# Kernel tuning notes

Hardware: AMD Instinct MI355X
Metric: run time of the kernel (lower is better)

The kernel has to match this reference:

```python
import jax, jax.numpy as jnp
import numpy as np

N_HEADS = 16
N_KV_HEADS = 4
HEAD_DIM = 64
ROPE_BASE = 10000.0

def _rope_cos_sin(T, dtype):
    # flash-attn style: cos/sin of shape [T, head_dim//2]
    inv_freq = 1.0 / (ROPE_BASE ** (jnp.arange(0, HEAD_DIM, 2, dtype=jnp.float32) / HEAD_DIM))
    freqs = jnp.arange(T, dtype=jnp.float32)[:, None] * inv_freq[None, :]  # [T, D/2]
    return jnp.cos(freqs).astype(dtype), jnp.sin(freqs).astype(dtype)

def _apply_rope(x, cos, sin):
    # x: [B, H, T, D], non-interleaved rotate-half on full head dim
    d2 = HEAD_DIM // 2
    x1, x2 = x[..., :d2], x[..., d2:]
    c = cos[None, None, :, :]
    s = sin[None, None, :, :]
    return jnp.concatenate([x1 * c - x2 * s, x2 * c + x1 * s], axis=-1)

def setup_inputs() -> dict:
    key = jax.random.key(0)
    ks = jax.random.split(key, 6)
    B, T, D = 1, 4096, 1024
    def g(k, shape, scale):
        return jax.random.normal(k, shape, dtype=jnp.float32) * scale
    return {
        "query": g(ks[0], (B, T, D), 1.0),
        "Wq": g(ks[1], (D, D), D ** -0.5),
        "Wk": g(ks[2], (D, N_KV_HEADS * HEAD_DIM), D ** -0.5),
        "Wv": g(ks[3], (D, N_KV_HEADS * HEAD_DIM), D ** -0.5),
        "W1": g(ks[4], (D, 4 * D), D ** -0.5),
        "W2": g(ks[5], (4 * D, D), (4 * D) ** -0.5),
    }

def reference(query, Wq, Wk, Wv, W1, W2):
    B, T, D = query.shape
    # QKV projections -> [B, H, T, Dh]
    q = (query @ Wq).reshape(B, T, N_HEADS, HEAD_DIM).transpose(0, 2, 1, 3)
    k = (query @ Wk).reshape(B, T, N_KV_HEADS, HEAD_DIM).transpose(0, 2, 1, 3)
    v = (query @ Wv).reshape(B, T, N_KV_HEADS, HEAD_DIM).transpose(0, 2, 1, 3)
    # RoPE (seqlen_offset = 0, no cache)
    cos, sin = _rope_cos_sin(T, q.dtype)
    q = _apply_rope(q, cos, sin)
    k = _apply_rope(k, cos, sin)
    # GQA: repeat KV heads to match Q heads
    n_rep = N_HEADS // N_KV_HEADS
    k = jnp.repeat(k, n_rep, axis=1)
    v = jnp.repeat(v, n_rep, axis=1)
    # Scaled dot-product attention, causal
    scale = HEAD_DIM ** -0.5
    scores = jnp.einsum("bhqd,bhkd->bhqk", q, k) * scale
    i = jnp.arange(T)[:, None]
    j = jnp.arange(T)[None, :]
    scores = jnp.where(j > i, jnp.finfo(scores.dtype).min, scores)
    attn = jax.nn.softmax(scores, axis=-1)
    out = jnp.einsum("bhqk,bhkd->bhqd", attn, v)  # [B, H, T, Dh]
    out = out.transpose(0, 2, 1, 3).reshape(B, T, D)
    # out_proj: Linear -> SiLU -> Linear (use_swiglu=True path)
    return jax.nn.silu(out @ W1) @ W2
```

## Files before the change

kernel.cpp:

```cpp
#include <hip/hip_runtime.h>
#include <stdint.h>

typedef unsigned short u16;
typedef __bf16 bf16x8 __attribute__((ext_vector_type(8)));
typedef float f32x4 __attribute__((ext_vector_type(4)));

#define T_SEQ 4096
#define DMODEL 1024

__device__ __forceinline__ float bf2f(u16 x) {
  union { uint32_t u; float f; } v; v.u = ((uint32_t)x) << 16; return v.f;
}
__device__ __forceinline__ u16 f2bf(float f) {
  union { float f; uint32_t u; } v; v.f = f;
  return (u16)((v.u + 0x7FFFu + ((v.u >> 16) & 1u)) >> 16);
}
__device__ __forceinline__ float fexp2(float x) {
#if __has_builtin(__builtin_amdgcn_exp2f)
  return __builtin_amdgcn_exp2f(x);
#else
  return __expf(x * 0.6931471805599453f);
#endif
}
__device__ __forceinline__ uint32_t pack_bf16(float lo, float hi) {
#if __has_builtin(__builtin_amdgcn_cvt_pk_bf16_f32)
  typedef __bf16 bf16x2_t __attribute__((ext_vector_type(2)));
  union { bf16x2_t v; uint32_t u; } c;
  c.v = __builtin_amdgcn_cvt_pk_bf16_f32(lo, hi);
  return c.u;
#else
  union { float f; uint32_t u; } a, b;
  a.f = lo; b.f = hi;
  return __builtin_amdgcn_perm(b.u + 0x8000u, a.u + 0x8000u, 0x07060302u);
#endif
}
__device__ __forceinline__ void async16(void* lds, const void* g) {
  __builtin_amdgcn_global_load_lds(
      (__attribute__((address_space(1))) void*)const_cast<void*>(g),
      (__attribute__((address_space(3))) void*)lds, 16, 0, 0);
}
__device__ __forceinline__ void storeC(u16* C, size_t i, float v) { C[i] = f2bf(v); }
__device__ __forceinline__ void storeC(float* C, size_t i, float v) { C[i] = v; }

__device__ __forceinline__ void wtrans_body(const float* __restrict__ in,
                                            u16* __restrict__ out, int K, int N,
                                            int bx, int by, int tid,
                                            float (*tile)[65]) {
  const int n0 = bx * 64, k0 = by * 64;
  const int r = tid >> 2, c = (tid & 3) * 16;
#pragma unroll
  for (int j = 0; j < 4; ++j) {
    float4 v = *(const float4*)&in[(size_t)(k0 + r) * N + n0 + c + j * 4];
    tile[r][c + j * 4 + 0] = v.x; tile[r][c + j * 4 + 1] = v.y;
    tile[r][c + j * 4 + 2] = v.z; tile[r][c + j * 4 + 3] = v.w;
  }
  __syncthreads();
  union { u16 s[16]; uint4 q[2]; } buf;
#pragma unroll
  for (int j = 0; j < 16; ++j) buf.s[j] = f2bf(tile[c + j][r]);
  u16* dst = out + (size_t)(n0 + r) * K + k0 + c;
  *(uint4*)(dst) = buf.q[0];
  *(uint4*)(dst + 8) = buf.q[1];
}

__global__ void __launch_bounds__(256) prep(const float* __restrict__ query,
                                            const float* __restrict__ Wq,
                                            const float* __restrict__ Wk,
                                            const float* __restrict__ Wv,
                                            const float* __restrict__ W1,
                                            const float* __restrict__ W2,
                                            u16* __restrict__ Xb,
                                            u16* __restrict__ WqkvT,
                                            u16* __restrict__ W1T,
                                            u16* __restrict__ W2T) {
  __shared__ float tile[64][65];
  const int b = blockIdx.x, tid = threadIdx.x;
  if (b < 4096) {
    int idx = (b * 256 + tid) * 4;
    float4 v = *(const float4*)(query + idx);
    union { u16 s[4]; uint2 q; } o;
    o.s[0] = f2bf(v.x); o.s[1] = f2bf(v.y); o.s[2] = f2bf(v.z); o.s[3] = f2bf(v.w);
    *(uint2*)(Xb + idx) = o.q;
  } else if (b < 4352) {
    int t = b - 4096;
    wtrans_body(Wq, WqkvT, 1024, 1024, t & 15, t >> 4, tid, tile);
  } else if (b < 4416) {
    int t = b - 4352;
    wtrans_body(Wk, WqkvT + (size_t)1024 * 1024, 1024, 256, t & 3, t >> 2, tid, tile);
  } else if (b < 4480) {
    int t = b - 4416;
    wtrans_body(Wv, WqkvT + (size_t)1280 * 1024, 1024, 256, t & 3, t >> 2, tid, tile);
  } else if (b < 5504) {
    int t = b - 4480;
    wtrans_body(W1, W1T, 1024, 4096, t & 63, t >> 6, tid, tile);
  } else {
    int t = b - 5504;
    wtrans_body(W2, W2T, 4096, 1024, t & 15, t >> 4, tid, tile);
  }
}

__global__ void __launch_bounds__(256) rope_vt(const u16* __restrict__ qkv,
                                               u16* __restrict__ Q,
                                               u16* __restrict__ Ko,
                                               u16* __restrict__ Vt) {
  __shared__ u16 tile[64][65];
  const int b = blockIdx.x, tid = threadIdx.x;
  if (b < 4096) {
    const int t = b;
    const int i = tid & 31;
    const float ang = (float)t * powf(10000.f, -(float)i * (1.f / 32.f));
    float s, c;
    sincosf(ang, &s, &c);
    const u16* row = qkv + (size_t)t * 1536;
    const float QS = 0.125f * 1.4426950408889634f;
    const float cq = c * QS, sq = s * QS;
#pragma unroll
    for (int it = 0; it < 2; ++it) {
      int h = (tid >> 5) + it * 8;
      float x1 = bf2f(row[h * 64 + i]);
      float x2 = bf2f(row[h * 64 + 32 + i]);
      size_t o = ((size_t)h * T_SEQ + t) * 64 + i;
      Q[o] = f2bf(x1 * cq - x2 * sq);
      Q[o + 32] = f2bf(x2 * cq + x1 * sq);
    }
    if (tid < 128) {
      int h = tid >> 5;
      float x1 = bf2f(row[1024 + h * 64 + i]);
      float x2 = bf2f(row[1024 + h * 64 + 32 + i]);
      size_t o = ((size_t)h * T_SEQ + t) * 64 + i;
      Ko[o] = f2bf(x1 * c - x2 * s);
      Ko[o + 32] = f2bf(x2 * c + x1 * s);
    }
  } else {
    const int t = b - 4096;
    const int t0 = (t & 63) * 64, h = t >> 6;
    const int r = tid >> 2, q4 = (tid & 3) * 16;
    const u16* src = qkv + (size_t)(t0 + r) * 1536 + 1280 + h * 64 + q4;
    union { u16 s[16]; uint4 q[2]; } buf;
    buf.q[0] = *(const uint4*)(src);
    buf.q[1] = *(const uint4*)(src + 8);
#pragma unroll
    for (int j = 0; j < 16; ++j) tile[r][q4 + j] = buf.s[j];
    __syncthreads();
#pragma unroll
    for (int j = 0; j < 16; ++j) buf.s[j] = tile[q4 + j][r];
    u16* dst = Vt + ((size_t)h * 64 + r) * T_SEQ + t0 + q4;
    *(uint4*)(dst) = buf.q[0];
    *(uint4*)(dst + 8) = buf.q[1];
  }
}

template <int AM, int ACT, typename OutT>
__global__ void __launch_bounds__(256) gemm_bt(const u16* __restrict__ A,
                                               const u16* __restrict__ Bt,
                                               OutT* __restrict__ C,
                                               int M, int N, int K) {
  __shared__ u16 sA[2][AM * 32][64];
  __shared__ u16 sB[2][128][64];
  const int tid = threadIdx.x;
  const int w = tid >> 6, lane = tid & 63;
  const int g = lane >> 4, l15 = lane & 15;
  const int r8 = lane >> 3, c8 = lane & 7;
  const int bm = blockIdx.y * (AM * 32), bn = blockIdx.x * 128;

  f32x4 acc[AM][4];
#pragma unroll
  for (int i = 0; i < AM; ++i)
#pragma unroll
    for (int j = 0; j < 4; ++j) acc[i][j] = (f32x4){0.f, 0.f, 0.f, 0.f};

  const u16* Ag = A + (size_t)(bm + w * (AM * 8) + r8) * K + (c8 ^ r8) * 8;
  const u16* Bg = Bt + (size_t)(bn + w * 32 + r8) * K + (c8 ^ r8) * 8;
  const int mrow = (w >> 1) * (AM * 16), ncol = (w & 1) * 64;
  const int swz = l15 & 7;

#define GSTAGE(K0, BUF)                                                        \
  {                                                                            \
    _Pragma("unroll") for (int t = 0; t < AM; ++t)                             \
      async16(&sA[BUF][w * (AM * 8) + t * 8][0], Ag + (size_t)(t * 8) * K + (K0)); \
    _Pragma("unroll") for (int t = 0; t < 4; ++t)                              \
      async16(&sB[BUF][w * 32 + t * 8][0], Bg + (size_t)(t * 8) * K + (K0));   \
  }

  GSTAGE(0, 0);
  int cur = 0;
  for (int k0 = 0; k0 < K; k0 += 64) {
    __syncthreads();
    if (k0 + 64 < K) GSTAGE(k0 + 64, cur ^ 1);
#pragma unroll
    for (int kk = 0; kk < 2; ++kk) {
      const int cb = ((kk * 4 + g) ^ swz) * 8;
      bf16x8 a[AM], b[4];
#pragma unroll
      for (int i = 0; i < AM; ++i) a[i] = *(const bf16x8*)&sA[cur][mrow + i * 16 + l15][cb];
#pragma unroll
      for (int i = 0; i < 4; ++i) b[i] = *(const bf16x8*)&sB[cur][ncol + i * 16 + l15][cb];
#pragma unroll
      for (int mi = 0; mi < AM; ++mi)
#pragma unroll
        for (int ni = 0; ni < 4; ++ni)
          acc[mi][ni] = __builtin_amdgcn_mfma_f32_16x16x32_bf16(a[mi], b[ni], acc[mi][ni], 0, 0, 0);
    }
    cur ^= 1;
  }
#undef GSTAGE
#pragma unroll
  for (int mi = 0; mi < AM; ++mi)
#pragma unroll
    for (int ni = 0; ni < 4; ++ni)
#pragma unroll
      for (int r = 0; r < 4; ++r) {
        int row = bm + mrow + mi * 16 + g * 4 + r;
        int col = bn + ncol + ni * 16 + l15;
        float v = acc[mi][ni][r];
        if (ACT == 1) v = v / (1.f + __expf(-v));
        storeC(C, (size_t)row * N + col, v);
      }
}

__global__ void __launch_bounds__(512, 2) gemm_ffn1(const u16* __restrict__ A,
                                                    const u16* __restrict__ Bt,
                                                    u16* __restrict__ C) {
  const int N = 4096, K = 1024;
  __shared__ u16 sA[2][256][64];
  __shared__ u16 sB[2][256][64];
  const int tid = threadIdx.x;
  const int w = tid >> 6, lane = tid & 63;
  const int g = lane >> 4, l15 = lane & 15;
  const int r8 = lane >> 3, c8 = lane & 7;
  const int wm = w >> 2, wn = w & 3;
  const int bm = blockIdx.y * 256, bn = blockIdx.x * 256;

  f32x4 acc[8][4];
#pragma unroll
  for (int i = 0; i < 8; ++i)
#pragma unroll
    for (int j = 0; j < 4; ++j) acc[i][j] = (f32x4){0.f, 0.f, 0.f, 0.f};

  const u16* Ag = A + (size_t)(bm + w * 32 + r8) * K + (c8 ^ r8) * 8;
  const u16* Bg = Bt + (size_t)(bn + w * 32 + r8) * K + (c8 ^ r8) * 8;
  const int mrow = wm * 128, ncol = wn * 64;
  const int swz = l15 & 7;

#define FSTAGE(K0, BUF)                                                   \
  {                                                                       \
    _Pragma("unroll") for (int t = 0; t < 4; ++t) {                       \
      async16(&sA[BUF][w * 32 + t * 8][0], Ag + (size_t)(t * 8) * K + (K0)); \
      async16(&sB[BUF][w * 32 + t * 8][0], Bg + (size_t)(t * 8) * K + (K0)); \
    }                                                                     \
  }

  FSTAGE(0, 0);
  int cur = 0;
  for (int k0 = 0; k0 < K; k0 += 64) {
    __syncthreads();
    if (k0 + 64 < K) FSTAGE(k0 + 64, cur ^ 1);
#pragma unroll
    for (int kk = 0; kk < 2; ++kk) {
      const int cb = ((kk * 4 + g) ^ swz) * 8;
      bf16x8 a[8], b[4];
#pragma unroll
      for (int i = 0; i < 8; ++i) a[i] = *(const bf16x8*)&sA[cur][mrow + i * 16 + l15][cb];
#pragma unroll
      for (int i = 0; i < 4; ++i) b[i] = *(const bf16x8*)&sB[cur][ncol + i * 16 + l15][cb];
#pragma unroll
      for (int mi = 0; mi < 8; ++mi)
#pragma unroll
        for (int ni = 0; ni < 4; ++ni)
          acc[mi][ni] = __builtin_amdgcn_mfma_f32_16x16x32_bf16(a[mi], b[ni], acc[mi][ni], 0, 0, 0);
    }
    cur ^= 1;
  }
#undef FSTAGE
#pragma unroll
  for (int mi = 0; mi < 8; ++mi)
#pragma unroll
    for (int ni = 0; ni < 4; ++ni)
#pragma unroll
      for (int r = 0; r < 4; ++r) {
        int row = bm + mrow + mi * 16 + g * 4 + r;
        int col = bn + ncol + ni * 16 + l15;
        float v = acc[mi][ni][r];
        v = v / (1.f + __expf(-v));
        C[(size_t)row * N + col] = f2bf(v);
      }
}

__global__ void __launch_bounds__(256, 2) gemm_w2(const u16* __restrict__ A,
                                                  const u16* __restrict__ Bt,
                                                  float* __restrict__ C0,
                                                  u16* __restrict__ C1) {
  __shared__ u16 sA[2][128][64];
  __shared__ u16 sB[2][128][64];
  const int K = 4096, N = 1024;
  const int z = blockIdx.z, koff = z * 2048;
  const int tid = threadIdx.x;
  const int w = tid >> 6, lane = tid & 63;
  const int g = lane >> 4, l15 = lane & 15;
  const int r8 = lane >> 3, c8 = lane & 7;
  const int bm = blockIdx.y * 128, bn = blockIdx.x * 128;

  f32x4 acc[4][4];
#pragma unroll
  for (int i = 0; i < 4; ++i)
#pragma unroll
    for (int j = 0; j < 4; ++j) acc[i][j] = (f32x4){0.f, 0.f, 0.f, 0.f};

  const u16* Ag = A + (size_t)(bm + w * 32 + r8) * K + koff + (c8 ^ r8) * 8;
  const u16* Bg = Bt + (size_t)(bn + w * 32 + r8) * K + koff + (c8 ^ r8) * 8;
  const int mrow = (w >> 1) * 64, ncol = (w & 1) * 64;
  const int swz = l15 & 7;

#define GSTAGE(K0, BUF)                                                   \
  {                                                                       \
    _Pragma("unroll") for (int t = 0; t < 4; ++t) {                       \
      async16(&sA[BUF][w * 32 + t * 8][0], Ag + (size_t)(t * 8) * K + (K0)); \
      async16(&sB[BUF][w * 32 + t * 8][0], Bg + (size_t)(t * 8) * K + (K0)); \
    }                                                                     \
  }

  GSTAGE(0, 0);
  int cur = 0;
  for (int k0 = 0; k0 < 2048; k0 += 64) {
    __syncthreads();
    if (k0 + 64 < 2048) GSTAGE(k0 + 64, cur ^ 1);
#pragma unroll
    for (int kk = 0; kk < 2; ++kk) {
      const int cb = ((kk * 4 + g) ^ swz) * 8;
      bf16x8 a[4], b[4];
#pragma unroll
      for (int i = 0; i < 4; ++i) {
        a[i] = *(const bf16x8*)&sA[cur][mrow + i * 16 + l15][cb];
        b[i] = *(const bf16x8*)&sB[cur][ncol + i * 16 + l15][cb];
      }
#pragma unroll
      for (int mi = 0; mi < 4; ++mi)
#pragma unroll
        for (int ni = 0; ni < 4; ++ni)
          acc[mi][ni] = __builtin_amdgcn_mfma_f32_16x16x32_bf16(a[mi], b[ni], acc[mi][ni], 0, 0, 0);
    }
    cur ^= 1;
  }
#undef GSTAGE
#pragma unroll
  for (int mi = 0; mi < 4; ++mi)
#pragma unroll
    for (int ni = 0; ni < 4; ++ni)
#pragma unroll
      for (int r = 0; r < 4; ++r) {
        size_t idx = (size_t)(bm + mrow + mi * 16 + g * 4 + r) * N + bn + ncol + ni * 16 + l15;
        if (z == 0) C0[idx] = acc[mi][ni][r];
        else        C1[idx] = f2bf(acc[mi][ni][r]);
      }
}

__global__ void __launch_bounds__(256) w2_combine(float* __restrict__ out,
                                                  const u16* __restrict__ P1) {
  int idx = (blockIdx.x * 256 + threadIdx.x) * 4;
  float4 v = *(const float4*)(out + idx);
  union { uint2 q; u16 s[4]; } p;
  p.q = *(const uint2*)(P1 + idx);
  v.x += bf2f(p.s[0]); v.y += bf2f(p.s[1]);
  v.z += bf2f(p.s[2]); v.w += bf2f(p.s[3]);
  *(float4*)(out + idx) = v;
}

__global__ void __launch_bounds__(256, 2) attn(const u16* __restrict__ Q,
                                               const u16* __restrict__ K,
                                               const u16* __restrict__ Vt,
                                               u16* __restrict__ O0,
                                               u16* __restrict__ O1,
                                               float* __restrict__ L0,
                                               float* __restrict__ L1) {
  __shared__ u16 sK[2][64][64];
  __shared__ u16 sV[3][64][64];
  __shared__ u16 sP[4][64][68];
  const int pr = blockIdx.x >> 1;
  const int split = blockIdx.x & 1;
  const int h = blockIdx.y;
  const int kvh = h >> 2;
  const int tid = threadIdx.x;
  const int w = tid >> 6, lane = tid & 63;
  const int g = lane >> 4, l15 = lane & 15;
  const int r8 = lane >> 3, c8 = lane & 7;
  const int swz = l15 & 7;
  const int t0 = pr, t1 = 31 - pr;
  const int off = split * 64;

  u16* Op = split ? O1 : O0;
  float* Lp = split ? L1 : L0;

  bf16x8 qf[2][2][2];
  {
    const u16* Qh = Q + (size_t)h * T_SEQ * 64;
#pragma unroll
    for (int half = 0; half < 2; ++half)
#pragma unroll
      for (int mi = 0; mi < 2; ++mi) {
        const int q = (half ? t1 : t0) * 128 + w * 32 + mi * 16 + l15;
#pragma unroll
        for (int kk = 0; kk < 2; ++kk)
          qf[half][mi][kk] = *(const bf16x8*)(Qh + (size_t)q * 64 + (kk * 4 + g) * 8);
      }
  }

  f32x4 oacc[2][2][4];
  f32x4 lacc[2][2];
#pragma unroll
  for (int half = 0; half < 2; ++half)
#pragma unroll
    for (int mi = 0; mi < 2; ++mi) {
      lacc[half][mi] = (f32x4){0.f, 0.f, 0.f, 0.f};
#pragma unroll
      for (int nd = 0; nd < 4; ++nd) oacc[half][mi][nd] = (f32x4){0.f, 0.f, 0.f, 0.f};
    }

  bf16x8 ONES;
  {
    union { u16 s[8]; bf16x8 v; } o;
#pragma unroll
    for (int i = 0; i < 8; ++i) o.s[i] = 0x3F80;
    ONES = o.v;
  }

  const u16* Kg = K + ((size_t)kvh * T_SEQ + w * 16 + r8) * 64 + (c8 ^ r8) * 8;
  const u16* Vg = Vt + ((size_t)kvh * 64 + w * 16 + r8) * T_SEQ + (c8 ^ r8) * 8;

  f32x4 s1[2][4], s0[2][4];
  uint2 pk1[2][4], pk0[2][4];

#define STAGE2(J, KB, VB)                                               \
  {                                                                     \
    const int kv0_ = (J) * 64;                                          \
    async16(&sK[KB][w * 16 + 0][0], Kg + (size_t)kv0_ * 64);            \
    async16(&sK[KB][w * 16 + 8][0], Kg + (size_t)(kv0_ + 8) * 64);      \
    async16(&sV[VB][w * 16 + 0][0], Vg + kv0_);                         \
    async16(&sV[VB][w * 16 + 8][0], Vg + (size_t)8 * T_SEQ + kv0_);     \
  }

#define QKMM(B, ACT0)                                                             \
  {                                                                               \
    _Pragma("unroll") for (int mi = 0; mi < 2; ++mi)                              \
    _Pragma("unroll") for (int kt = 0; kt < 4; ++kt) {                            \
      s1[mi][kt] = (f32x4){0.f, 0.f, 0.f, 0.f};                                   \
      if (ACT0) s0[mi][kt] = (f32x4){0.f, 0.f, 0.f, 0.f};                         \
    }                                                                             \
    __builtin_amdgcn_s_setprio(1);                                                \
    _Pragma("unroll") for (int kt = 0; kt < 4; ++kt)                              \
    _Pragma("unroll") for (int kk = 0; kk < 2; ++kk) {                            \
      bf16x8 kf = *(const bf16x8*)&sK[B][kt * 16 + l15][((kk * 4 + g) ^ swz) * 8]; \
      _Pragma("unroll") for (int mi = 0; mi < 2; ++mi) {                          \
        s1[mi][kt] = __builtin_amdgcn_mfma_f32_16x16x32_bf16(kf, qf[1][mi][kk], s1[mi][kt], 0, 0, 0); \
        if (ACT0)                                                                 \
          s0[mi][kt] = __builtin_amdgcn_mfma_f32_16x16x32_bf16(kf, qf[0][mi][kk], s0[mi][kt], 0, 0, 0); \
      }                                                                           \
    }                                                                             \
    __builtin_amdgcn_s_setprio(0);                                                \
  }

#define PVL(PACT0, VB)                                                            \
  {                                                                               \
    __builtin_amdgcn_s_setprio(1);                                                \
    _Pragma("unroll") for (int kk = 0; kk < 2; ++kk) {                            \
      bf16x8 pf1[2], pf0[2];                                                      \
      _Pragma("unroll") for (int mi = 0; mi < 2; ++mi) {                          \
        pf1[mi] = *(const bf16x8*)&sP[w][32 + mi * 16 + l15][kk * 32 + g * 8];    \
        if (PACT0) pf0[mi] = *(const bf16x8*)&sP[w][mi * 16 + l15][kk * 32 + g * 8]; \
      }                                                                           \
      _Pragma("unroll") for (int mi = 0; mi < 2; ++mi) {                          \
        lacc[1][mi] = __builtin_amdgcn_mfma_f32_16x16x32_bf16(pf1[mi], ONES, lacc[1][mi], 0, 0, 0); \
        if (PACT0)                                                                \
          lacc[0][mi] = __builtin_amdgcn_mfma_f32_16x16x32_bf16(pf0[mi], ONES, lacc[0][mi], 0, 0, 0); \
      }                                                                           \
      _Pragma("unroll") for (int nd = 0; nd < 4; ++nd) {                          \
        bf16x8 vf = *(const bf16x8*)&sV[VB][nd * 16 + l15][((kk * 4 + g) ^ swz) * 8]; \
        _Pragma("unroll") for (int mi = 0; mi < 2; ++mi) {                        \
          oacc[1][mi][nd] = __builtin_amdgcn_mfma_f32_16x16x32_bf16(pf1[mi], vf, oacc[1][mi][nd], 0, 0, 0); \
          if (PACT0)                                                              \
            oacc[0][mi][nd] = __builtin_amdgcn_mfma_f32_16x16x32_bf16(pf0[mi], vf, oacc[0][mi][nd], 0, 0, 0); \
        }                                                                         \
      }                                                                           \
    }                                                                             \
    __builtin_amdgcn_s_setprio(0);                                                \
  }

#define EXPPK(ACT0, M0, M1)                                                       \
  {                                                                               \
    _Pragma("unroll") for (int mi = 0; mi < 2; ++mi) {                            \
      const int thr_ = w * 32 + mi * 16 + l15 - off;                              \
      _Pragma("unroll") for (int kt = 0; kt < 4; ++kt) {                          \
        float p_[4];                                                              \
        _Pragma("unroll") for (int r = 0; r < 4; ++r) {                           \
          float p = fexp2(s1[mi][kt][r]);                                         \
          if (M1 && (kt * 16 + g * 4 + r > thr_)) p = 0.f;                        \
          p_[r] = p;                                                              \
        }                                                                         \
        pk1[mi][kt].x = pack_bf16(p_[0], p_[1]);                                  \
        pk1[mi][kt].y = pack_bf16(p_[2], p_[3]);                                  \
        if (ACT0) {                                                               \
          float q_[4];                                                            \
          _Pragma("unroll") for (int r = 0; r < 4; ++r) {                         \
            float p = fexp2(s0[mi][kt][r]);                                       \
            if (M0 && (kt * 16 + g * 4 + r > thr_)) p = 0.f;                      \
            q_[r] = p;                                                            \
          }                                                                       \
          pk0[mi][kt].x = pack_bf16(q_[0], q_[1]);                                \
          pk0[mi][kt].y = pack_bf16(q_[2], q_[3]);                                \
        }                                                                         \
      }                                                                           \
    }                                                                             \
  }

#define SPW(ACT0)                                                                 \
  {                                                                               \
    _Pragma("unroll") for (int mi = 0; mi < 2; ++mi)                              \
    _Pragma("unroll") for (int kt = 0; kt < 4; ++kt) {                            \
      *(uint2*)&sP[w][32 + mi * 16 + l15][kt * 16 + g * 4] = pk1[mi][kt];         \
      if (ACT0) *(uint2*)&sP[w][mi * 16 + l15][kt * 16 + g * 4] = pk0[mi][kt];    \
    }                                                                             \
  }

  STAGE2(split, 0, 0);
  __syncthreads();
  STAGE2(split + 2, 1, 1);
  QKMM(0, true);
  if (t0 == 0) { EXPPK(true, true, false); }
  else         { EXPPK(true, false, false); }
  SPW(true);
  int b = 1;
  int vp = 0, vc = 1, vn = 2;
  int i = 1;
  for (; i < t0; ++i) {
    __syncthreads();
    STAGE2(split + 2 * (i + 1), b ^ 1, vn);
    QKMM(b, true);
    PVL(true, vp);
    EXPPK(true, false, false);
    __builtin_amdgcn_wave_barrier();
    SPW(true);
    b ^= 1; int tmp = vp; vp = vc; vc = vn; vn = tmp;
  }
  if (t0 >= 1) {
    __syncthreads();
    STAGE2(split + 2 * (i + 1), b ^ 1, vn);
    QKMM(b, true);
    PVL(true, vp);
    EXPPK(true, true, false);
    __builtin_amdgcn_wave_barrier();
    SPW(true);
    b ^= 1; int tmp = vp; vp = vc; vc = vn; vn = tmp;
    ++i;
  }
  if (i < t1) {
    __syncthreads();
    STAGE2(split + 2 * (i + 1), b ^ 1, vn);
    QKMM(b, false);
    PVL(true, vp);
    EXPPK(false, false, false);
    __builtin_amdgcn_wave_barrier();
    SPW(false);
    b ^= 1; { int tmp = vp; vp = vc; vc = vn; vn = tmp; }
    ++i;
    for (; i < t1; ++i) {
      __syncthreads();
      STAGE2(split + 2 * (i + 1), b ^ 1, vn);
      QKMM(b, false);
      PVL(false, vp);
      EXPPK(false, false, false);
      __builtin_amdgcn_wave_barrier();
      SPW(false);
      b ^= 1; int tmp = vp; vp = vc; vc = vn; vn = tmp;
    }
    __syncthreads();
    QKMM(b, false);
    PVL(false, vp);
    EXPPK(false, false, true);
    __builtin_amdgcn_wave_barrier();
    SPW(false);
    __builtin_amdgcn_wave_barrier();
    PVL(false, vc);
  } else {
    __syncthreads();
    QKMM(b, false);
    PVL(true, vp);
    EXPPK(false, false, true);
    __builtin_amdgcn_wave_barrier();
    SPW(false);
    __builtin_amdgcn_wave_barrier();
    PVL(false, vc);
  }
#undef STAGE2
#undef QKMM
#undef PVL
#undef EXPPK
#undef SPW

#pragma unroll
  for (int half = 0; half < 2; ++half) {
    const int tb = (half ? t1 : t0) * 128;
#pragma unroll
    for (int mi = 0; mi < 2; ++mi)
#pragma unroll
      for (int r = 0; r < 4; ++r) {
        const int trow = tb + w * 32 + mi * 16 + g * 4 + r;
#pragma unroll
        for (int nd = 0; nd < 4; ++nd)
          Op[(size_t)trow * DMODEL + h * 64 + nd * 16 + l15] = f2bf(oacc[half][mi][nd][r]);
        if (l15 == 0) Lp[h * T_SEQ + trow] = lacc[half][mi][r];
      }
  }
}

__global__ void __launch_bounds__(256) attn_combine(const u16* __restrict__ O0,
                                                    const u16* __restrict__ O1,
                                                    const float* __restrict__ L0,
                                                    const float* __restrict__ L1,
                                                    u16* __restrict__ AO) {
  const int t = blockIdx.x, tid = threadIdx.x;
  const int h = tid >> 4, d4 = (tid & 15) * 4;
  const float inv = 1.f / (L0[h * T_SEQ + t] + L1[h * T_SEQ + t]);
  const size_t idx = (size_t)t * DMODEL + h * 64 + d4;
  union { uint2 q; u16 s[4]; } a, b, o;
  a.q = *(const uint2*)(O0 + idx);
  b.q = *(const uint2*)(O1 + idx);
#pragma unroll
  for (int i = 0; i < 4; ++i) o.s[i] = f2bf((bf2f(a.s[i]) + bf2f(b.s[i])) * inv);
  *(uint2*)(AO + idx) = o.q;
}

extern "C" void kernel_launch(void* const* d_in, const int* in_sizes, int n_in,
                              void* d_out, int out_size, void* d_ws, size_t ws_size,
                              hipStream_t stream) {
  const float* query = (const float*)d_in[0];
  const float* Wq = (const float*)d_in[1];
  const float* Wk = (const float*)d_in[2];
  const float* Wv = (const float*)d_in[3];
  const float* W1 = (const float*)d_in[4];
  const float* W2 = (const float*)d_in[5];
  float* out = (float*)d_out;

  char* ws = (char*)d_ws;
  size_t off = 0;
  auto alloc = [&](size_t bytes) { char* p = ws + off; off += (bytes + 255) & ~(size_t)255; return p; };
  u16* Xb   = (u16*)alloc((size_t)4096 * 1024 * 2);
  u16* QKVb = (u16*)alloc((size_t)4096 * 1536 * 2);
  u16* Qb   = (u16*)alloc((size_t)16 * 4096 * 64 * 2);
  u16* Kb   = (u16*)alloc((size_t)4 * 4096 * 64 * 2);
  u16* Vtb  = (u16*)alloc((size_t)4 * 4096 * 64 * 2);
  u16* H    = (u16*)ws;
  u16*   O0p = Xb;
  u16*   O1p = QKVb;
  float* L0p = (float*)(QKVb + (size_t)4096 * 1024);
  float* L1p = L0p + 16 * T_SEQ;
  u16* WqkvT = (u16*)alloc((size_t)1536 * 1024 * 2);
  u16* W1T   = (u16*)alloc((size_t)4096 * 1024 * 2);
  u16* W2T   = (u16*)alloc((size_t)1024 * 4096 * 2);
  u16* AO    = (u16*)alloc((size_t)4096 * 1024 * 2);
  u16* P1    = W1T;
  (void)ws_size; (void)in_sizes; (void)n_in; (void)out_size;

  prep<<<6528, 256, 0, stream>>>(query, Wq, Wk, Wv, W1, W2, Xb, WqkvT, W1T, W2T);
  gemm_bt<2, 0, u16><<<dim3(12, 64), 256, 0, stream>>>(Xb, WqkvT, QKVb, 4096, 1536, 1024);
  rope_vt<<<4352, 256, 0, stream>>>(QKVb, Qb, Kb, Vtb);
  attn<<<dim3(32, 16), 256, 0, stream>>>(Qb, Kb, Vtb, O0p, O1p, L0p, L1p);
  attn_combine<<<4096, 256, 0, stream>>>(O0p, O1p, L0p, L1p, AO);
  gemm_ffn1<<<dim3(16, 16), 512, 0, stream>>>(AO, W1T, H);
  gemm_w2<<<dim3(8, 32, 2), 256, 0, stream>>>(H, W2T, out, P1);
  w2_combine<<<4096, 256, 0, stream>>>(out, P1);
}
```

Baseline: 278.1 us.

## Load K tiles directly into registers instead of staging through LDS

The attention kernel no longer stages K through a double-buffered shared-memory tile. Each wave now loads its K MFMA fragments straight from global memory into registers, issuing the next tile's load right after the current QK matmul as a register-level prefetch. This removes LDS writes and reads for K and frees shared memory. In exchange every wave fetches the full K tile itself (four times the global/L2 traffic per block), and the extra 8 bf16x8 registers may raise register pressure.

```diff
diff --git a/kernel.cpp b/kernel.cpp
--- a/kernel.cpp
+++ b/kernel.cpp
@@ -372,7 +372,6 @@
                                                u16* __restrict__ O1,
                                                float* __restrict__ L0,
                                                float* __restrict__ L1) {
-  __shared__ u16 sK[2][64][64];
   __shared__ u16 sV[3][64][64];
   __shared__ u16 sP[4][64][68];
   const int pr = blockIdx.x >> 1;
@@ -423,22 +422,29 @@
     ONES = o.v;
   }
 
-  const u16* Kg = K + ((size_t)kvh * T_SEQ + w * 16 + r8) * 64 + (c8 ^ r8) * 8;
+  const u16* Kd = K + ((size_t)kvh * T_SEQ + l15) * 64 + g * 8;
   const u16* Vg = Vt + ((size_t)kvh * 64 + w * 16 + r8) * T_SEQ + (c8 ^ r8) * 8;
 
+  bf16x8 kfr[4][2];
   f32x4 s1[2][4], s0[2][4];
   uint2 pk1[2][4], pk0[2][4];
 
-#define STAGE2(J, KB, VB)                                               \
+#define KLOAD(J)                                                        \
   {                                                                     \
     const int kv0_ = (J) * 64;                                          \
-    async16(&sK[KB][w * 16 + 0][0], Kg + (size_t)kv0_ * 64);            \
-    async16(&sK[KB][w * 16 + 8][0], Kg + (size_t)(kv0_ + 8) * 64);      \
+    _Pragma("unroll") for (int kt = 0; kt < 4; ++kt)                    \
+    _Pragma("unroll") for (int kk = 0; kk < 2; ++kk)                    \
+      kfr[kt][kk] = *(const bf16x8*)(Kd + (size_t)(kv0_ + kt * 16) * 64 + kk * 32); \
+  }
+
+#define STAGEV(J, VB)                                                   \
+  {                                                                     \
+    const int kv0_ = (J) * 64;                                          \
     async16(&sV[VB][w * 16 + 0][0], Vg + kv0_);                         \
     async16(&sV[VB][w * 16 + 8][0], Vg + (size_t)8 * T_SEQ + kv0_);     \
   }
 
-#define QKMM(B, ACT0)                                                             \
+#define QKMM(ACT0)                                                                \
   {                                                                               \
     _Pragma("unroll") for (int mi = 0; mi < 2; ++mi)                              \
     _Pragma("unroll") for (int kt = 0; kt < 4; ++kt) {                            \
@@ -448,11 +454,10 @@
     __builtin_amdgcn_s_setprio(1);                                                \
     _Pragma("unroll") for (int kt = 0; kt < 4; ++kt)                              \
     _Pragma("unroll") for (int kk = 0; kk < 2; ++kk) {                            \
-      bf16x8 kf = *(const bf16x8*)&sK[B][kt * 16 + l15][((kk * 4 + g) ^ swz) * 8]; \
       _Pragma("unroll") for (int mi = 0; mi < 2; ++mi) {                          \
-        s1[mi][kt] = __builtin_amdgcn_mfma_f32_16x16x32_bf16(kf, qf[1][mi][kk], s1[mi][kt], 0, 0, 0); \
+        s1[mi][kt] = __builtin_amdgcn_mfma_f32_16x16x32_bf16(kfr[kt][kk], qf[1][mi][kk], s1[mi][kt], 0, 0, 0); \
         if (ACT0)                                                                 \
-          s0[mi][kt] = __builtin_amdgcn_mfma_f32_16x16x32_bf16(kf, qf[0][mi][kk], s0[mi][kt], 0, 0, 0); \
+          s0[mi][kt] = __builtin_amdgcn_mfma_f32_16x16x32_bf16(kfr[kt][kk], qf[0][mi][kk], s0[mi][kt], 0, 0, 0); \
       }                                                                           \
     }                                                                             \
     __builtin_amdgcn_s_setprio(0);                                                \
@@ -520,59 +525,63 @@
     }                                                                             \
   }
 
-  STAGE2(split, 0, 0);
-  __syncthreads();
-  STAGE2(split + 2, 1, 1);
-  QKMM(0, true);
+  KLOAD(split);
+  STAGEV(split, 0);
+  STAGEV(split + 2, 1);
+  QKMM(true);
+  KLOAD(split + 2);
   if (t0 == 0) { EXPPK(true, true, false); }
   else         { EXPPK(true, false, false); }
   SPW(true);
-  int b = 1;
   int vp = 0, vc = 1, vn = 2;
   int i = 1;
   for (; i < t0; ++i) {
     __syncthreads();
-    STAGE2(split + 2 * (i + 1), b ^ 1, vn);
-    QKMM(b, true);
+    STAGEV(split + 2 * (i + 1), vn);
+    QKMM(true);
+    KLOAD(split + 2 * (i + 1));
     PVL(true, vp);
     EXPPK(true, false, false);
     __builtin_amdgcn_wave_barrier();
     SPW(true);
-    b ^= 1; int tmp = vp; vp = vc; vc = vn; vn = tmp;
+    int tmp = vp; vp = vc; vc = vn; vn = tmp;
   }
   if (t0 >= 1) {
     __syncthreads();
-    STAGE2(split + 2 * (i + 1), b ^ 1, vn);
-    QKMM(b, true);
+    STAGEV(split + 2 * (i + 1), vn);
+    QKMM(true);
+    KLOAD(split + 2 * (i + 1));
     PVL(true, vp);
     EXPPK(true, true, false);
     __builtin_amdgcn_wave_barrier();
     SPW(true);
-    b ^= 1; int tmp = vp; vp = vc; vc = vn; vn = tmp;
+    int tmp = vp; vp = vc; vc = vn; vn = tmp;
     ++i;
   }
   if (i < t1) {
     __syncthreads();
-    STAGE2(split + 2 * (i + 1), b ^ 1, vn);
-    QKMM(b, false);
+    STAGEV(split + 2 * (i + 1), vn);
+    QKMM(false);
+    KLOAD(split + 2 * (i + 1));
     PVL(true, vp);
     EXPPK(false, false, false);
     __builtin_amdgcn_wave_barrier();
     SPW(false);
-    b ^= 1; { int tmp = vp; vp = vc; vc = vn; vn = tmp; }
+    { int tmp = vp; vp = vc; vc = vn; vn = tmp; }
     ++i;
     for (; i < t1; ++i) {
       __syncthreads();
-      STAGE2(split + 2 * (i + 1), b ^ 1, vn);
-      QKMM(b, false);
+      STAGEV(split + 2 * (i + 1), vn);
+      QKMM(false);
+      KLOAD(split + 2 * (i + 1));
       PVL(false, vp);
       EXPPK(false, false, false);
       __builtin_amdgcn_wave_barrier();
       SPW(false);
-      b ^= 1; int tmp = vp; vp = vc; vc = vn; vn = tmp;
+      int tmp = vp; vp = vc; vc = vn; vn = tmp;
     }
     __syncthreads();
-    QKMM(b, false);
+    QKMM(false);
     PVL(false, vp);
     EXPPK(false, false, true);
     __builtin_amdgcn_wave_barrier();
@@ -581,7 +590,7 @@
     PVL(false, vc);
   } else {
     __syncthreads();
-    QKMM(b, false);
+    QKMM(false);
     PVL(true, vp);
     EXPPK(false, false, true);
     __builtin_amdgcn_wave_barrier();
@@ -589,7 +598,8 @@
     __builtin_amdgcn_wave_barrier();
     PVL(false, vc);
   }
-#undef STAGE2
+#undef KLOAD
+#undef STAGEV
 #undef QKMM
 #undef PVL
 #undef EXPPK
```

Measured after the change: 301.9 us. +8.6%, slower.
